# Kernel optimization log

Hardware: AMD Instinct MI355X
Metric: run time of the kernel (lower is better)

## Reference

```python
import jax, jax.numpy as jnp
import numpy as np
import math

H = 8
D_MODEL = 512
D_K = D_MODEL // H
NEG = -1.0e9


def setup_inputs() -> dict:
    key = jax.random.key(0)
    ks = jax.random.split(key, 10)
    B, S, D = 8, 1024, D_MODEL
    s = 1.0 / math.sqrt(D)
    return {
        "query": jax.random.normal(ks[0], (B, S, D), jnp.float32),
        "key": jax.random.normal(ks[1], (B, S, D), jnp.float32),
        "value": jax.random.normal(ks[2], (B, S, D), jnp.float32),
        "group_prob": jax.random.uniform(ks[3], (B, S, S), jnp.float32),
        "Wq": jax.random.normal(ks[4], (D, D), jnp.float32) * s,
        "Wk": jax.random.normal(ks[5], (D, D), jnp.float32) * s,
        "Wv": jax.random.normal(ks[6], (D, D), jnp.float32) * s,
        "Wh": jax.random.normal(ks[7], (D, D), jnp.float32) * s,
        "bh": jax.random.normal(ks[8], (D,), jnp.float32) * s,
        "mask": jax.random.randint(ks[9], (B, S, S), 0, 2, jnp.int32),
    }


def reference(query, key, value, group_prob, Wq, Wk, Wv, Wh, bh, mask):
    B, S, D = query.shape
    # project and split heads: [B, H, S, d_k]
    def split(x, W):
        return (x @ W.T).reshape(B, S, H, D_K).transpose(0, 2, 1, 3)
    q, k, v = split(query, Wq), split(key, Wk), split(value, Wv)
    scores = jnp.einsum('bhqd,bhkd->bhqk', q, k) / jnp.sqrt(jnp.asarray(D_K, q.dtype))
    # masked_fill where (mask | eye) == 0, i.e. keep mask-allowed or diagonal positions
    eye = jnp.eye(S, dtype=jnp.int32)
    allowed = (mask[:, None, :, :] | eye[None, None, :, :]) != 0  # [B,1,S,S]
    scores = jnp.where(allowed, scores, jnp.asarray(NEG, scores.dtype))
    p_attn = jax.nn.softmax(scores, axis=-1)
    p_attn = p_attn * group_prob[:, None, :, :]  # post-softmax group scaling
    x = jnp.einsum('bhqk,bhkd->bhqd', p_attn, v)
    x = x.transpose(0, 2, 1, 3).reshape(B, S, D)
    return x @ Wh.T + bh
```

## Files before the change

kernel.cpp:

```cpp
#include <hip/hip_runtime.h>
#include <hip/hip_bf16.h>
#include <cstdint>


typedef __attribute__((ext_vector_type(8))) short short8;
typedef __attribute__((ext_vector_type(4))) float f32x4;

__device__ __forceinline__ ushort f2bf(float x) {
    union { __hip_bfloat16 h; ushort u; } v;
    v.h = __float2bfloat16(x);
    return v.u;
}
__device__ __forceinline__ float bf2f(ushort u) {
    union { uint u; float f; } v; v.u = ((uint)u) << 16; return v.f;
}
__device__ __forceinline__ uint cvtpk(float lo, float hi) {
    uint r;
    asm("v_cvt_pk_bf16_f32 %0, %1, %2" : "=v"(r) : "v"(lo), "v"(hi));
    return r;
}
__device__ __forceinline__ f32x4 mfma16(short8 a, short8 b, f32x4 c) {
    return __builtin_amdgcn_mfma_f32_16x16x32_bf16(a, b, c, 0, 0, 0);
}
__device__ __forceinline__ void gl16(const void* g, const void* l) {
    __builtin_amdgcn_global_load_lds(
        (const __attribute__((address_space(1))) uint32_t*)(uintptr_t)g,
        (__attribute__((address_space(3))) uint32_t*)(uint32_t)(uintptr_t)l,
        16, 0, 0);
}

__global__ __launch_bounds__(256)
void prep(const float* __restrict__ q, const float* __restrict__ k,
          const float* __restrict__ v,
          const float* __restrict__ wq, const float* __restrict__ wk,
          const float* __restrict__ wv, const float* __restrict__ wh,
          const int* __restrict__ mask, const float* __restrict__ gp,
          ushort* __restrict__ qb, ushort* __restrict__ kb,
          ushort* __restrict__ vb,
          ushort* __restrict__ wqb, ushort* __restrict__ wkb,
          ushort* __restrict__ wvb, ushort* __restrict__ whb,
          ushort* __restrict__ gmb)
{
    const int bid = blockIdx.x, tid = threadIdx.x;
    if (bid < 8192) {
        size_t i = ((size_t)bid * 256 + tid) * 4;
        int4 m = *(const int4*)(mask + i);
        float4 gg = *(const float4*)(gp + i);
        int kk = (int)(i & 1023), qq = (int)((i >> 10) & 1023);
        uint u01 = cvtpk(gg.x, gg.y), u23 = cvtpk(gg.z, gg.w);
        ushort4 o;
        o.x = (m.x != 0 || qq == kk + 0) ? (ushort)(u01 & 0xffff) : (ushort)0xBF80;
        o.y = (m.y != 0 || qq == kk + 1) ? (ushort)(u01 >> 16)    : (ushort)0xBF80;
        o.z = (m.z != 0 || qq == kk + 2) ? (ushort)(u23 & 0xffff) : (ushort)0xBF80;
        o.w = (m.w != 0 || qq == kk + 3) ? (ushort)(u23 >> 16)    : (ushort)0xBF80;
        *(ushort4*)(gmb + i) = o;
    } else if (bid < 20480) {
        size_t id = ((size_t)(bid - 8192) * 256 + tid) * 4;
        int t = (int)(id >> 22);
        size_t off = id & 4194303;
        const float* s = (t == 0) ? q : (t == 1) ? k : v;
        ushort* d = (t == 0) ? qb : (t == 1) ? kb : vb;
        float4 x = *(const float4*)(s + off);
        uint2 o; o.x = cvtpk(x.x, x.y); o.y = cvtpk(x.z, x.w);
        *(uint2*)(d + off) = o;
    } else {
        size_t id = ((size_t)(bid - 20480) * 256 + tid) * 4;
        int t = (int)(id >> 18);
        size_t off = id & 262143;
        const float* s = (t == 0) ? wq : (t == 1) ? wk : (t == 2) ? wv : wh;
        ushort* d = (t == 0) ? wqb : (t == 1) ? wkb : (t == 2) ? wvb : whb;
        float4 x = *(const float4*)(s + off);
        uint2 o; o.x = cvtpk(x.x, x.y); o.y = cvtpk(x.z, x.w);
        *(uint2*)(d + off) = o;
    }
}

__global__ __launch_bounds__(256, 2)
void gemm3(const ushort* __restrict__ qb, const ushort* __restrict__ kb,
           const ushort* __restrict__ vb,
           const ushort* __restrict__ Wqb, const ushort* __restrict__ Wkb,
           const ushort* __restrict__ Wvb,
           ushort* __restrict__ q_ws, ushort* __restrict__ k_ws,
           ushort* __restrict__ vT)
{
    __shared__ __attribute__((aligned(16))) ushort As[8192];
    __shared__ __attribute__((aligned(16))) ushort Bs[8192];

    const int z = blockIdx.z;
    const ushort* A = (z == 0) ? qb : (z == 1) ? kb : Wvb;
    const ushort* B = (z == 0) ? Wqb : (z == 1) ? Wkb : vb;
    const int mt = (z == 2) ? blockIdx.y : blockIdx.x;
    const int nt = (z == 2) ? blockIdx.x : blockIdx.y;
    const int m0 = mt * 128, n0 = nt * 128;
    const int tid = threadIdx.x, lane = tid & 63, wave = tid >> 6;
    const int l15 = lane & 15, g = lane >> 4;
    const int wm = wave >> 1, wn = wave & 1;

    const int cb = (lane & 7) << 4;
    int soff[4];
    #pragma unroll
    for (int it = 0; it < 4; ++it) {
        int r = (it * 4 + wave) * 8 + (lane >> 3);
        soff[it] = r * 1024 + (cb ^ ((r & 7) << 4));
    }
    const char* Ab = (const char*)A + (size_t)m0 * 1024;
    const char* Bb = (const char*)B + (size_t)n0 * 1024;

    const int sw = (l15 & 7) << 4;
    const int c0 = (g * 16) ^ sw;
    const int c1 = (64 + g * 16) ^ sw;

    f32x4 acc[4][4];
    #pragma unroll
    for (int i = 0; i < 4; ++i)
        #pragma unroll
        for (int j = 0; j < 4; ++j) acc[i][j] = (f32x4){0.f, 0.f, 0.f, 0.f};

    for (int ks = 0; ks < 8; ++ks) {
        const int kof = ks * 128;
        #pragma unroll
        for (int it = 0; it < 4; ++it) {
            gl16(Ab + soff[it] + kof, (const char*)As + (it * 4 + wave) * 1024);
            gl16(Bb + soff[it] + kof, (const char*)Bs + (it * 4 + wave) * 1024);
        }
        __syncthreads();
        #pragma unroll
        for (int kk = 0; kk < 2; ++kk) {
            const int cc = kk ? c1 : c0;
            short8 af[4], bf[4];
            #pragma unroll
            for (int i = 0; i < 4; ++i)
                af[i] = *(const short8*)((const char*)As + (wm * 64 + i * 16 + l15) * 128 + cc);
            #pragma unroll
            for (int j = 0; j < 4; ++j)
                bf[j] = *(const short8*)((const char*)Bs + (wn * 64 + j * 16 + l15) * 128 + cc);
            #pragma unroll
            for (int i = 0; i < 4; ++i)
                #pragma unroll
                for (int j = 0; j < 4; ++j)
                    acc[i][j] = mfma16(af[i], bf[j], acc[i][j]);
        }
        __syncthreads();
    }

    #pragma unroll
    for (int i = 0; i < 4; ++i) {
        #pragma unroll
        for (int j = 0; j < 4; ++j) {
            #pragma unroll
            for (int r = 0; r < 4; ++r) {
                int mm = m0 + wm * 64 + i * 16 + g * 4 + r;
                int nn = n0 + wn * 64 + j * 16 + l15;
                float val = acc[i][j][r];
                if (z == 0) {
                    val *= 0.18033688f;
                    int b = mm >> 10, s = mm & 1023, h = nn >> 6, dk = nn & 63;
                    q_ws[((((size_t)(b * 8 + h)) << 10) + s) * 64 + dk] = f2bf(val);
                } else if (z == 1) {
                    int b = mm >> 10, s = mm & 1023, h = nn >> 6, dk = nn & 63;
                    k_ws[((((size_t)(b * 8 + h)) << 10) + s) * 64 + dk] = f2bf(val);
                } else {
                    int h = mm >> 6, d = mm & 63, b = nn >> 10, s = nn & 1023;
                    vT[(((size_t)(b * 8 + h) * 64 + d) << 10) + s] = f2bf(val);
                }
            }
        }
    }
}

__global__ __launch_bounds__(256, 2)
void gemm_o(const ushort* __restrict__ Xh, const ushort* __restrict__ Whb,
            const float* __restrict__ bias, float* __restrict__ out)
{
    __shared__ __attribute__((aligned(16))) ushort As[8192];
    __shared__ __attribute__((aligned(16))) ushort Bs[8192];

    const int m0 = blockIdx.x * 128, n0 = blockIdx.y * 128;
    const int tid = threadIdx.x, lane = tid & 63, wave = tid >> 6;
    const int l15 = lane & 15, g = lane >> 4;
    const int wm = wave >> 1, wn = wave & 1;
    const int bb = m0 >> 10, s0 = m0 & 1023;

    const int cb = (lane & 7) << 4;
    int aoff[4], boff[4];
    #pragma unroll
    for (int it = 0; it < 4; ++it) {
        int r = (it * 4 + wave) * 8 + (lane >> 3);
        int swz = cb ^ ((r & 7) << 4);
        aoff[it] = ((bb * 8) * 1024 + s0 + r) * 128 + swz;
        boff[it] = (n0 + r) * 1024 + swz;
    }
    const int sw = (l15 & 7) << 4;
    const int c0 = (g * 16) ^ sw;
    const int c1 = (64 + g * 16) ^ sw;

    f32x4 acc[4][4];
    #pragma unroll
    for (int i = 0; i < 4; ++i)
        #pragma unroll
        for (int j = 0; j < 4; ++j) acc[i][j] = (f32x4){0.f, 0.f, 0.f, 0.f};

    for (int ks = 0; ks < 8; ++ks) {
        #pragma unroll
        for (int it = 0; it < 4; ++it) {
            gl16((const char*)Xh + aoff[it] + ks * 131072,
                 (const char*)As + (it * 4 + wave) * 1024);
            gl16((const char*)Whb + boff[it] + ks * 128,
                 (const char*)Bs + (it * 4 + wave) * 1024);
        }
        __syncthreads();
        #pragma unroll
        for (int kk = 0; kk < 2; ++kk) {
            const int cc = kk ? c1 : c0;
            short8 af[4], bf[4];
            #pragma unroll
            for (int i = 0; i < 4; ++i)
                af[i] = *(const short8*)((const char*)As + (wm * 64 + i * 16 + l15) * 128 + cc);
            #pragma unroll
            for (int j = 0; j < 4; ++j)
                bf[j] = *(const short8*)((const char*)Bs + (wn * 64 + j * 16 + l15) * 128 + cc);
            #pragma unroll
            for (int i = 0; i < 4; ++i)
                #pragma unroll
                for (int j = 0; j < 4; ++j)
                    acc[i][j] = mfma16(af[i], bf[j], acc[i][j]);
        }
        __syncthreads();
    }

    float bv[4];
    #pragma unroll
    for (int j = 0; j < 4; ++j) bv[j] = bias[n0 + wn * 64 + j * 16 + l15];

    #pragma unroll
    for (int i = 0; i < 4; ++i)
        #pragma unroll
        for (int j = 0; j < 4; ++j)
            #pragma unroll
            for (int r = 0; r < 4; ++r) {
                int mm = m0 + wm * 64 + i * 16 + g * 4 + r;
                int nn = n0 + wn * 64 + j * 16 + l15;
                out[(size_t)mm * 512 + nn] = acc[i][j][r] + bv[j];
            }
}

__global__ __launch_bounds__(256, 2)
void attn(const ushort* __restrict__ Qh, const ushort* __restrict__ Kh,
          const ushort* __restrict__ Vt, const ushort* __restrict__ gm,
          ushort* __restrict__ xo)
{
    __shared__ __attribute__((aligned(16))) ushort kv[2][2][4096];

    const int w = blockIdx.x;
    const int bh = w & 63, qt = w >> 6;
    const int tid = threadIdx.x, wave = tid >> 6, lane = tid & 63;
    const int l15 = lane & 15, g = lane >> 4;
    const int q0 = qt * 128 + wave * 32;
    const int b = bh >> 3;

    const char* Kpb = (const char*)(Kh + (size_t)bh * 65536);
    const char* Vpb = (const char*)(Vt + (size_t)bh * 65536);
    const ushort* QpA = Qh + ((size_t)bh * 1024 + q0 + l15) * 64;
    const ushort* QpB = QpA + 16 * 64;
    const ushort* gmpA = gm + ((size_t)b * 1024 + q0 + l15) * 1024;
    const ushort* gmpB = gmpA + 16 * 1024;

    const short8 qa0 = *(const short8*)(QpA + g * 8);
    const short8 qa1 = *(const short8*)(QpA + 32 + g * 8);
    const short8 qb0 = *(const short8*)(QpB + g * 8);
    const short8 qb1 = *(const short8*)(QpB + 32 + g * 8);

    const int cb = (lane & 7) << 4;
    const int rA = wave * 8 + (lane >> 3);
    const int rB = rA + 32;
    const int gkA = (rA & 3) + 4 * ((rA >> 4) & 1) + 8 * ((rA >> 2) & 3) + 32 * (rA >> 5);
    const int gkB = (rB & 3) + 4 * ((rB >> 4) & 1) + 8 * ((rB >> 2) & 3) + 32 * (rB >> 5);
    const int okA = gkA * 128 + (cb ^ ((rA & 7) << 4));
    const int okB = gkB * 128 + (cb ^ ((rB & 7) << 4));
    const int ovA = rA * 2048 + (cb ^ ((rA & 7) << 4));
    const int ovB = rB * 2048 + (cb ^ ((rB & 7) << 4));

    const int sw = (l15 & 7) << 4;
    const int c0 = (g * 16) ^ sw;
    const int c1 = (64 + g * 16) ^ sw;

    f32x4 otA[4], otB[4];
    #pragma unroll
    for (int t = 0; t < 4; ++t) {
        otA[t] = (f32x4){0.f, 0.f, 0.f, 0.f};
        otB[t] = (f32x4){0.f, 0.f, 0.f, 0.f};
    }
    float lsA = 0.f, lsB = 0.f;

    gl16(Kpb + okA, &kv[0][0][wave * 512]);
    gl16(Kpb + okB, &kv[0][0][(4 + wave) * 512]);
    gl16(Vpb + ovA, &kv[0][1][wave * 512]);
    gl16(Vpb + ovB, &kv[0][1][(4 + wave) * 512]);
    short8 gcA0 = *(const short8*)(gmpA + g * 8);
    short8 gcA1 = *(const short8*)(gmpA + 32 + g * 8);
    short8 gcB0 = *(const short8*)(gmpB + g * 8);
    short8 gcB1 = *(const short8*)(gmpB + 32 + g * 8);
    __syncthreads();

    for (int t = 0; t < 16; ++t) {
        const int cur = t & 1;
        short8 gnA0, gnA1, gnB0, gnB1;
        if (t < 15) {
            const char* kp = Kpb + (size_t)(t + 1) * 8192;
            const char* vp = Vpb + (size_t)(t + 1) * 128;
            gl16(kp + okA, &kv[cur ^ 1][0][wave * 512]);
            gl16(kp + okB, &kv[cur ^ 1][0][(4 + wave) * 512]);
            gl16(vp + ovA, &kv[cur ^ 1][1][wave * 512]);
            gl16(vp + ovB, &kv[cur ^ 1][1][(4 + wave) * 512]);
            gnA0 = *(const short8*)(gmpA + (t + 1) * 64 + g * 8);
            gnA1 = *(const short8*)(gmpA + (t + 1) * 64 + 32 + g * 8);
            gnB0 = *(const short8*)(gmpB + (t + 1) * 64 + g * 8);
            gnB1 = *(const short8*)(gmpB + (t + 1) * 64 + 32 + g * 8);
        }
        const char* kbuf = (const char*)&kv[cur][0][0];
        const char* vbuf = (const char*)&kv[cur][1][0];

        f32x4 sA[4], sB[4];
        #pragma unroll
        for (int t4 = 0; t4 < 4; ++t4) {
            const char* ka = kbuf + (t4 * 16 + l15) * 128;
            short8 k0f = *(const short8*)(ka + c0);
            short8 k1f = *(const short8*)(ka + c1);
            f32x4 za = (f32x4){0.f, 0.f, 0.f, 0.f};
            za = mfma16(k0f, qa0, za);
            za = mfma16(k1f, qa1, za);
            sA[t4] = za;
            f32x4 zb = (f32x4){0.f, 0.f, 0.f, 0.f};
            zb = mfma16(k0f, qb0, zb);
            zb = mfma16(k1f, qb1, zb);
            sB[t4] = zb;
        }

        union { uint4 u; short8 s; } paA0, paA1, paB0, paB1;
        {
            float p[16], gv[16];
            #pragma unroll
            for (int c = 0; c < 2; ++c) {
                const short8 gc = c ? gcA1 : gcA0;
                #pragma unroll
                for (int j = 0; j < 8; ++j) {
                    const int jj = c * 8 + j;
                    const int t4 = 2 * c + (j >> 2), r = j & 3;
                    float gvv = bf2f((ushort)gc[j]);
                    gv[jj] = gvv;
                    p[jj] = exp2f((gvv >= 0.f) ? sA[t4][r] : -1.0e9f);
                }
            }
            lsA += (((p[0] + p[1]) + (p[2] + p[3])) + ((p[4] + p[5]) + (p[6] + p[7])))
                 + (((p[8] + p[9]) + (p[10] + p[11])) + ((p[12] + p[13]) + (p[14] + p[15])));
            paA0.u.x = cvtpk(p[0] * gv[0],  p[1] * gv[1]);
            paA0.u.y = cvtpk(p[2] * gv[2],  p[3] * gv[3]);
            paA0.u.z = cvtpk(p[4] * gv[4],  p[5] * gv[5]);
            paA0.u.w = cvtpk(p[6] * gv[6],  p[7] * gv[7]);
            paA1.u.x = cvtpk(p[8] * gv[8],  p[9] * gv[9]);
            paA1.u.y = cvtpk(p[10] * gv[10], p[11] * gv[11]);
            paA1.u.z = cvtpk(p[12] * gv[12], p[13] * gv[13]);
            paA1.u.w = cvtpk(p[14] * gv[14], p[15] * gv[15]);
        }
        {
            float p[16], gv[16];
            #pragma unroll
            for (int c = 0; c < 2; ++c) {
                const short8 gc = c ? gcB1 : gcB0;
                #pragma unroll
                for (int j = 0; j < 8; ++j) {
                    const int jj = c * 8 + j;
                    const int t4 = 2 * c + (j >> 2), r = j & 3;
                    float gvv = bf2f((ushort)gc[j]);
                    gv[jj] = gvv;
                    p[jj] = exp2f((gvv >= 0.f) ? sB[t4][r] : -1.0e9f);
                }
            }
            lsB += (((p[0] + p[1]) + (p[2] + p[3])) + ((p[4] + p[5]) + (p[6] + p[7])))
                 + (((p[8] + p[9]) + (p[10] + p[11])) + ((p[12] + p[13]) + (p[14] + p[15])));
            paB0.u.x = cvtpk(p[0] * gv[0],  p[1] * gv[1]);
            paB0.u.y = cvtpk(p[2] * gv[2],  p[3] * gv[3]);
            paB0.u.z = cvtpk(p[4] * gv[4],  p[5] * gv[5]);
            paB0.u.w = cvtpk(p[6] * gv[6],  p[7] * gv[7]);
            paB1.u.x = cvtpk(p[8] * gv[8],  p[9] * gv[9]);
            paB1.u.y = cvtpk(p[10] * gv[10], p[11] * gv[11]);
            paB1.u.z = cvtpk(p[12] * gv[12], p[13] * gv[13]);
            paB1.u.w = cvtpk(p[14] * gv[14], p[15] * gv[15]);
        }

        #pragma unroll
        for (int td = 0; td < 4; ++td) {
            const char* va = vbuf + (td * 16 + l15) * 128;
            short8 v0 = *(const short8*)(va + c0);
            short8 v1 = *(const short8*)(va + c1);
            otA[td] = mfma16(v0, paA0.s, otA[td]);
            otA[td] = mfma16(v1, paA1.s, otA[td]);
            otB[td] = mfma16(v0, paB0.s, otB[td]);
            otB[td] = mfma16(v1, paB1.s, otB[td]);
        }
        __syncthreads();
        if (t < 15) { gcA0 = gnA0; gcA1 = gnA1; gcB0 = gnB0; gcB1 = gnB1; }
    }

    lsA += __shfl_xor(lsA, 16, 64);
    lsA += __shfl_xor(lsA, 32, 64);
    lsB += __shfl_xor(lsB, 16, 64);
    lsB += __shfl_xor(lsB, 32, 64);
    const float invA = 1.0f / lsA;
    const float invB = 1.0f / lsB;

    ushort* xpA = xo + ((size_t)bh * 1024 + q0 + l15) * 64;
    ushort* xpB = xpA + 16 * 64;
    #pragma unroll
    for (int td = 0; td < 4; ++td) {
        uint2 oa, ob;
        oa.x = cvtpk(otA[td][0] * invA, otA[td][1] * invA);
        oa.y = cvtpk(otA[td][2] * invA, otA[td][3] * invA);
        ob.x = cvtpk(otB[td][0] * invB, otB[td][1] * invB);
        ob.y = cvtpk(otB[td][2] * invB, otB[td][3] * invB);
        *(uint2*)(xpA + td * 16 + g * 4) = oa;
        *(uint2*)(xpB + td * 16 + g * 4) = ob;
    }
}

extern "C" void kernel_launch(void* const* d_in, const int* in_sizes, int n_in,
                              void* d_out, int out_size, void* d_ws, size_t ws_size,
                              hipStream_t stream)
{
    const float* query = (const float*)d_in[0];
    const float* key   = (const float*)d_in[1];
    const float* value = (const float*)d_in[2];
    const float* gprob = (const float*)d_in[3];
    const float* Wq    = (const float*)d_in[4];
    const float* Wk    = (const float*)d_in[5];
    const float* Wv    = (const float*)d_in[6];
    const float* Wh    = (const float*)d_in[7];
    const float* bh    = (const float*)d_in[8];
    const int*   mask  = (const int*)d_in[9];
    float* out = (float*)d_out;

    ushort* ws = (ushort*)d_ws;
    const size_t HS = (size_t)64 * 65536;
    ushort* q_ws = ws;
    ushort* k_ws = ws + HS;
    ushort* vT   = ws + 2 * HS;
    ushort* gmb  = ws + 3 * HS;
    ushort* qb   = ws + 5 * HS;
    ushort* kb   = ws + 6 * HS;
    ushort* vb   = ws + 7 * HS;
    ushort* wqb  = ws + 8 * HS;
    ushort* wkb  = wqb + 262144;
    ushort* wvb  = wkb + 262144;
    ushort* whb  = wvb + 262144;
    ushort* x_ws = qb;

    prep<<<21504, 256, 0, stream>>>(query, key, value, Wq, Wk, Wv, Wh,
                                    mask, gprob, qb, kb, vb,
                                    wqb, wkb, wvb, whb, gmb);
    gemm3<<<dim3(64, 4, 3), 256, 0, stream>>>(qb, kb, vb, wqb, wkb, wvb,
                                              q_ws, k_ws, vT);
    attn<<<512, 256, 0, stream>>>(q_ws, k_ws, vT, gmb, x_ws);
    gemm_o<<<dim3(64, 4), 256, 0, stream>>>(x_ws, whb, bh, out);
}
```

Measured before the change: 101.8 us.

## Fuse mask and group-prob reads into attention kernel, drop bf16 pre-pack pass

Removes the prep pass that packed the int32 mask and fp32 group_prob into one bf16 tensor with a sentinel for masked slots. The attention kernel now loads mask and group_prob directly and applies the mask and diagonal test inline. This saves the write and re-read of the packed intermediate. In exchange, attention reads 8 bytes per element instead of 2, and does so once per head. The previous one-iteration register prefetch of those values is also gone, so load latency may be more exposed.

```diff
diff --git a/kernel.cpp b/kernel.cpp
--- a/kernel.cpp
+++ b/kernel.cpp
@@ -10,9 +10,6 @@
     union { __hip_bfloat16 h; ushort u; } v;
     v.h = __float2bfloat16(x);
     return v.u;
-}
-__device__ __forceinline__ float bf2f(ushort u) {
-    union { uint u; float f; } v; v.u = ((uint)u) << 16; return v.f;
 }
 __device__ __forceinline__ uint cvtpk(float lo, float hi) {
     uint r;
@@ -29,33 +26,36 @@
         16, 0, 0);
 }
 
+__device__ __forceinline__ void ld16i(const int* p, int (&d)[16]) {
+    int4 a = *(const int4*)p,       b = *(const int4*)(p + 4);
+    int4 c = *(const int4*)(p + 32), e = *(const int4*)(p + 36);
+    d[0]=a.x; d[1]=a.y; d[2]=a.z;  d[3]=a.w;
+    d[4]=b.x; d[5]=b.y; d[6]=b.z;  d[7]=b.w;
+    d[8]=c.x; d[9]=c.y; d[10]=c.z; d[11]=c.w;
+    d[12]=e.x; d[13]=e.y; d[14]=e.z; d[15]=e.w;
+}
+__device__ __forceinline__ void ld16f(const float* p, float (&d)[16]) {
+    float4 a = *(const float4*)p,        b = *(const float4*)(p + 4);
+    float4 c = *(const float4*)(p + 32), e = *(const float4*)(p + 36);
+    d[0]=a.x; d[1]=a.y; d[2]=a.z;  d[3]=a.w;
+    d[4]=b.x; d[5]=b.y; d[6]=b.z;  d[7]=b.w;
+    d[8]=c.x; d[9]=c.y; d[10]=c.z; d[11]=c.w;
+    d[12]=e.x; d[13]=e.y; d[14]=e.z; d[15]=e.w;
+}
+
 __global__ __launch_bounds__(256)
 void prep(const float* __restrict__ q, const float* __restrict__ k,
           const float* __restrict__ v,
           const float* __restrict__ wq, const float* __restrict__ wk,
           const float* __restrict__ wv, const float* __restrict__ wh,
-          const int* __restrict__ mask, const float* __restrict__ gp,
           ushort* __restrict__ qb, ushort* __restrict__ kb,
           ushort* __restrict__ vb,
           ushort* __restrict__ wqb, ushort* __restrict__ wkb,
-          ushort* __restrict__ wvb, ushort* __restrict__ whb,
-          ushort* __restrict__ gmb)
+          ushort* __restrict__ wvb, ushort* __restrict__ whb)
 {
     const int bid = blockIdx.x, tid = threadIdx.x;
-    if (bid < 8192) {
-        size_t i = ((size_t)bid * 256 + tid) * 4;
-        int4 m = *(const int4*)(mask + i);
-        float4 gg = *(const float4*)(gp + i);
-        int kk = (int)(i & 1023), qq = (int)((i >> 10) & 1023);
-        uint u01 = cvtpk(gg.x, gg.y), u23 = cvtpk(gg.z, gg.w);
-        ushort4 o;
-        o.x = (m.x != 0 || qq == kk + 0) ? (ushort)(u01 & 0xffff) : (ushort)0xBF80;
-        o.y = (m.y != 0 || qq == kk + 1) ? (ushort)(u01 >> 16)    : (ushort)0xBF80;
-        o.z = (m.z != 0 || qq == kk + 2) ? (ushort)(u23 & 0xffff) : (ushort)0xBF80;
-        o.w = (m.w != 0 || qq == kk + 3) ? (ushort)(u23 >> 16)    : (ushort)0xBF80;
-        *(ushort4*)(gmb + i) = o;
-    } else if (bid < 20480) {
-        size_t id = ((size_t)(bid - 8192) * 256 + tid) * 4;
+    if (bid < 12288) {
+        size_t id = ((size_t)bid * 256 + tid) * 4;
         int t = (int)(id >> 22);
         size_t off = id & 4194303;
         const float* s = (t == 0) ? q : (t == 1) ? k : v;
@@ -64,7 +64,7 @@
         uint2 o; o.x = cvtpk(x.x, x.y); o.y = cvtpk(x.z, x.w);
         *(uint2*)(d + off) = o;
     } else {
-        size_t id = ((size_t)(bid - 20480) * 256 + tid) * 4;
+        size_t id = ((size_t)(bid - 12288) * 256 + tid) * 4;
         int t = (int)(id >> 18);
         size_t off = id & 262143;
         const float* s = (t == 0) ? wq : (t == 1) ? wk : (t == 2) ? wv : wh;
@@ -244,10 +244,34 @@
             }
 }
 
+__device__ __forceinline__ void softmax_direct(
+    const int (&mm)[16], const float (&gv)[16], int dq,
+    const f32x4 (&s4)[4], float& lsum, uint4& u0, uint4& u1)
+{
+    float p[16];
+    #pragma unroll
+    for (int jj = 0; jj < 16; ++jj) {
+        const int kof = (jj & 7) + ((jj >> 3) << 5);
+        const int t4 = ((jj >> 3) << 1) + ((jj & 7) >> 2), r = jj & 3;
+        const bool allowed = (mm[jj] != 0) || (kof == dq);
+        p[jj] = exp2f(allowed ? s4[t4][r] : -1.0e9f);
+    }
+    lsum += (((p[0] + p[1]) + (p[2] + p[3])) + ((p[4] + p[5]) + (p[6] + p[7])))
+          + (((p[8] + p[9]) + (p[10] + p[11])) + ((p[12] + p[13]) + (p[14] + p[15])));
+    u0.x = cvtpk(p[0] * gv[0],  p[1] * gv[1]);
+    u0.y = cvtpk(p[2] * gv[2],  p[3] * gv[3]);
+    u0.z = cvtpk(p[4] * gv[4],  p[5] * gv[5]);
+    u0.w = cvtpk(p[6] * gv[6],  p[7] * gv[7]);
+    u1.x = cvtpk(p[8] * gv[8],  p[9] * gv[9]);
+    u1.y = cvtpk(p[10] * gv[10], p[11] * gv[11]);
+    u1.z = cvtpk(p[12] * gv[12], p[13] * gv[13]);
+    u1.w = cvtpk(p[14] * gv[14], p[15] * gv[15]);
+}
+
 __global__ __launch_bounds__(256, 2)
 void attn(const ushort* __restrict__ Qh, const ushort* __restrict__ Kh,
-          const ushort* __restrict__ Vt, const ushort* __restrict__ gm,
-          ushort* __restrict__ xo)
+          const ushort* __restrict__ Vt, const int* __restrict__ mask,
+          const float* __restrict__ gp, ushort* __restrict__ xo)
 {
     __shared__ __attribute__((aligned(16))) ushort kv[2][2][4096];
 
@@ -262,8 +286,13 @@
     const char* Vpb = (const char*)(Vt + (size_t)bh * 65536);
     const ushort* QpA = Qh + ((size_t)bh * 1024 + q0 + l15) * 64;
     const ushort* QpB = QpA + 16 * 64;
-    const ushort* gmpA = gm + ((size_t)b * 1024 + q0 + l15) * 1024;
-    const ushort* gmpB = gmpA + 16 * 1024;
+
+    const int qrowA = q0 + l15;
+    const size_t mbaseA = (((size_t)(b << 10) + qrowA) << 10) + g * 8;
+    const int*   mA = mask + mbaseA;
+    const int*   mB = mA + 16384;
+    const float* gA = gp + mbaseA;
+    const float* gB = gA + 16384;
 
     const short8 qa0 = *(const short8*)(QpA + g * 8);
     const short8 qa1 = *(const short8*)(QpA + 32 + g * 8);
@@ -296,15 +325,17 @@
     gl16(Kpb + okB, &kv[0][0][(4 + wave) * 512]);
     gl16(Vpb + ovA, &kv[0][1][wave * 512]);
     gl16(Vpb + ovB, &kv[0][1][(4 + wave) * 512]);
-    short8 gcA0 = *(const short8*)(gmpA + g * 8);
-    short8 gcA1 = *(const short8*)(gmpA + 32 + g * 8);
-    short8 gcB0 = *(const short8*)(gmpB + g * 8);
-    short8 gcB1 = *(const short8*)(gmpB + 32 + g * 8);
     __syncthreads();
 
     for (int t = 0; t < 16; ++t) {
         const int cur = t & 1;
-        short8 gnA0, gnA1, gnB0, gnB1;
+        int   mmA[16], mmB[16];
+        float gvA[16], gvB[16];
+        ld16i(mA + t * 64, mmA);
+        ld16f(gA + t * 64, gvA);
+        ld16i(mB + t * 64, mmB);
+        ld16f(gB + t * 64, gvB);
+
         if (t < 15) {
             const char* kp = Kpb + (size_t)(t + 1) * 8192;
             const char* vp = Vpb + (size_t)(t + 1) * 128;
@@ -312,10 +343,6 @@
             gl16(kp + okB, &kv[cur ^ 1][0][(4 + wave) * 512]);
             gl16(vp + ovA, &kv[cur ^ 1][1][wave * 512]);
             gl16(vp + ovB, &kv[cur ^ 1][1][(4 + wave) * 512]);
-            gnA0 = *(const short8*)(gmpA + (t + 1) * 64 + g * 8);
-            gnA1 = *(const short8*)(gmpA + (t + 1) * 64 + 32 + g * 8);
-            gnB0 = *(const short8*)(gmpB + (t + 1) * 64 + g * 8);
-            gnB1 = *(const short8*)(gmpB + (t + 1) * 64 + 32 + g * 8);
         }
         const char* kbuf = (const char*)&kv[cur][0][0];
         const char* vbuf = (const char*)&kv[cur][1][0];
@@ -336,57 +363,12 @@
             sB[t4] = zb;
         }
 
+        const int dqA = qrowA - t * 64 - g * 8;
+        const int dqB = dqA + 16;
+
         union { uint4 u; short8 s; } paA0, paA1, paB0, paB1;
-        {
-            float p[16], gv[16];
-            #pragma unroll
-            for (int c = 0; c < 2; ++c) {
-                const short8 gc = c ? gcA1 : gcA0;
-                #pragma unroll
-                for (int j = 0; j < 8; ++j) {
-                    const int jj = c * 8 + j;
-                    const int t4 = 2 * c + (j >> 2), r = j & 3;
-                    float gvv = bf2f((ushort)gc[j]);
-                    gv[jj] = gvv;
-                    p[jj] = exp2f((gvv >= 0.f) ? sA[t4][r] : -1.0e9f);
-                }
-            }
-            lsA += (((p[0] + p[1]) + (p[2] + p[3])) + ((p[4] + p[5]) + (p[6] + p[7])))
-                 + (((p[8] + p[9]) + (p[10] + p[11])) + ((p[12] + p[13]) + (p[14] + p[15])));
-            paA0.u.x = cvtpk(p[0] * gv[0],  p[1] * gv[1]);
-            paA0.u.y = cvtpk(p[2] * gv[2],  p[3] * gv[3]);
-            paA0.u.z = cvtpk(p[4] * gv[4],  p[5] * gv[5]);
-            paA0.u.w = cvtpk(p[6] * gv[6],  p[7] * gv[7]);
-            paA1.u.x = cvtpk(p[8] * gv[8],  p[9] * gv[9]);
-            paA1.u.y = cvtpk(p[10] * gv[10], p[11] * gv[11]);
-            paA1.u.z = cvtpk(p[12] * gv[12], p[13] * gv[13]);
-            paA1.u.w = cvtpk(p[14] * gv[14], p[15] * gv[15]);
-        }
-        {
-            float p[16], gv[16];
-            #pragma unroll
-            for (int c = 0; c < 2; ++c) {
-                const short8 gc = c ? gcB1 : gcB0;
-                #pragma unroll
-                for (int j = 0; j < 8; ++j) {
-                    const int jj = c * 8 + j;
-                    const int t4 = 2 * c + (j >> 2), r = j & 3;
-                    float gvv = bf2f((ushort)gc[j]);
-                    gv[jj] = gvv;
-                    p[jj] = exp2f((gvv >= 0.f) ? sB[t4][r] : -1.0e9f);
-                }
-            }
-            lsB += (((p[0] + p[1]) + (p[2] + p[3])) + ((p[4] + p[5]) + (p[6] + p[7])))
-                 + (((p[8] + p[9]) + (p[10] + p[11])) + ((p[12] + p[13]) + (p[14] + p[15])));
-            paB0.u.x = cvtpk(p[0] * gv[0],  p[1] * gv[1]);
-            paB0.u.y = cvtpk(p[2] * gv[2],  p[3] * gv[3]);
-            paB0.u.z = cvtpk(p[4] * gv[4],  p[5] * gv[5]);
-            paB0.u.w = cvtpk(p[6] * gv[6],  p[7] * gv[7]);
-            paB1.u.x = cvtpk(p[8] * gv[8],  p[9] * gv[9]);
-            paB1.u.y = cvtpk(p[10] * gv[10], p[11] * gv[11]);
-            paB1.u.z = cvtpk(p[12] * gv[12], p[13] * gv[13]);
-            paB1.u.w = cvtpk(p[14] * gv[14], p[15] * gv[15]);
-        }
+        softmax_direct(mmA, gvA, dqA, sA, lsA, paA0.u, paA1.u);
+        softmax_direct(mmB, gvB, dqB, sB, lsB, paB0.u, paB1.u);
 
         #pragma unroll
         for (int td = 0; td < 4; ++td) {
@@ -399,7 +381,6 @@
             otB[td] = mfma16(v1, paB1.s, otB[td]);
         }
         __syncthreads();
-        if (t < 15) { gcA0 = gnA0; gcA1 = gnA1; gcB0 = gnB0; gcB1 = gnB1; }
     }
 
     lsA += __shfl_xor(lsA, 16, 64);
@@ -444,7 +425,6 @@
     ushort* q_ws = ws;
     ushort* k_ws = ws + HS;
     ushort* vT   = ws + 2 * HS;
-    ushort* gmb  = ws + 3 * HS;
     ushort* qb   = ws + 5 * HS;
     ushort* kb   = ws + 6 * HS;
     ushort* vb   = ws + 7 * HS;
@@ -454,11 +434,10 @@
     ushort* whb  = wvb + 262144;
     ushort* x_ws = qb;
 
-    prep<<<21504, 256, 0, stream>>>(query, key, value, Wq, Wk, Wv, Wh,
-                                    mask, gprob, qb, kb, vb,
-                                    wqb, wkb, wvb, whb, gmb);
+    prep<<<13312, 256, 0, stream>>>(query, key, value, Wq, Wk, Wv, Wh,
+                                    qb, kb, vb, wqb, wkb, wvb, whb);
     gemm3<<<dim3(64, 4, 3), 256, 0, stream>>>(qb, kb, vb, wqb, wkb, wvb,
                                               q_ws, k_ws, vT);
-    attn<<<512, 256, 0, stream>>>(q_ws, k_ws, vT, gmb, x_ws);
+    attn<<<512, 256, 0, stream>>>(q_ws, k_ws, vT, mask, gprob, x_ws);
     gemm_o<<<dim3(64, 4), 256, 0, stream>>>(x_ws, whb, bh, out);
 }
```

After: 129.6 us. +27.4%, slower.
